# Kernel tuning notes

Hardware: AMD Instinct MI355X
Metric: run time of the kernel (lower is better)

The kernel has to match this reference:

```python
import jax, jax.numpy as jnp
import numpy as np

B, S, D = 4, 2048, 1024

def setup_inputs() -> dict:
    key = jax.random.key(0)
    k1, k2, k3, k4 = jax.random.split(key, 4)
    scale = 1.0 / np.sqrt(D)
    return {
        "X": jax.random.normal(k1, (B, S, D), dtype=jnp.float32),
        "W_Q": jax.random.normal(k2, (D, D), dtype=jnp.float32) * scale,
        "W_K": jax.random.normal(k3, (D, D), dtype=jnp.float32) * scale,
        "W_V": jax.random.normal(k4, (D, D), dtype=jnp.float32) * scale,
    }

def reference(X, W_Q, W_K, W_V):
    # nn.Linear computes X @ W.T; weights stored as [out, in]
    Q = jnp.einsum('bsd,ed->bse', X, W_Q)
    K = jnp.einsum('bsd,ed->bse', X, W_K)
    V = jnp.einsum('bsd,ed->bse', X, W_V)
    d_model = X.shape[-1]
    scores = jnp.einsum('bqd,bkd->bqk', Q, K) / jnp.sqrt(jnp.float32(d_model))
    S_len = X.shape[1]
    causal = jnp.tril(jnp.ones((S_len, S_len), dtype=bool))  # True = keep
    scores = jnp.where(causal[None, :, :], scores, -jnp.inf)
    attn = jax.nn.softmax(scores, axis=-1)
    return jnp.einsum('bqk,bkd->bqd', attn, V)
```

## Files before the change

### kernel.cpp

```cpp
#include <hip/hip_runtime.h>

typedef unsigned short u16;
typedef __attribute__((ext_vector_type(8))) short short8;
typedef __attribute__((ext_vector_type(4))) float floatx4;
typedef __attribute__((ext_vector_type(4))) unsigned short ushortx4;

#define BATCH 4
#define SEQ   2048
#define DMODEL 1024

__device__ __forceinline__ u16 f2bf(float f) {
  unsigned int u = __builtin_bit_cast(unsigned int, f);
  u = (u + 0x7FFFu + ((u >> 16) & 1u)) >> 16;
  return (u16)u;
}

typedef const __attribute__((address_space(1))) unsigned int as1_u32;
typedef __attribute__((address_space(3))) unsigned int as3_u32;

__device__ __forceinline__ void gload16(const void* gp, void* lp) {
  __builtin_amdgcn_global_load_lds((as1_u32*)gp, (as3_u32*)lp, 16, 0, 0);
}

#define CFENCE asm volatile("" ::: "memory")
#define LGKM0  do { asm volatile("s_waitcnt lgkmcnt(0)" ::: "memory"); \
                    __builtin_amdgcn_sched_barrier(0); } while (0)

template<int NW, int STRIPE>
__device__ __forceinline__ void stage_unit(
    const u16* __restrict__ G, int ld, int org, int kt, int h,
    u16* region, int w, int l)
{
  constexpr int CPS = STRIPE / 16;
  const int lr = l >> 3, s = l & 7;
  #pragma unroll
  for (int i = 0; i < 2; ++i) {
    int c = i * NW + w;
    int R = (c / CPS) * STRIPE + h * (STRIPE / 2) + (c % CPS) * 8;
    const u16* src = G + (size_t)(org + R + lr) * ld + kt * 64 + ((s ^ lr) << 3);
    gload16(src, region + R * 64);
  }
}

template<int REP>
__device__ __forceinline__ short8 rdfrag(const u16* region, int wq, int m, int kh, int l) {
  int r = wq * (REP * 16) + m * 16 + (l & 15);
  int c = kh * 32 + ((l >> 4) << 3);
  return *(const short8*)(region + ((r * 64 + c) ^ ((r & 7) << 3)));
}

template<int WM, int WN, int MREP, int NREP>
__device__ __forceinline__ void gemm_core(
    const u16* __restrict__ A, int lda,
    const u16* __restrict__ B, int ldb,
    int m0, int n0, int NT, u16* lds,
    floatx4 (&acc)[MREP][NREP])
{
  constexpr int NW = WM * WN;
  constexpr int BM = WM * MREP * 16, BN = WN * NREP * 16;
  constexpr int ABUF = BM * 64;
  constexpr int BUFSZ = (BM + BN) * 64;
  constexpr int MH = MREP / 2, NH = NREP / 2;
  constexpr int SA = BM / WM, SB = BN / WN;

  const int tid = threadIdx.x;
  const int w = tid >> 6, l = tid & 63;
  const int wr = w / WN, wc = w % WN;

  u16* buf0 = lds;
  u16* buf1 = lds + BUFSZ;

  stage_unit<NW, SA>(A, lda, m0, 0, 0, buf0, w, l);
  stage_unit<NW, SB>(B, ldb, n0, 0, 0, buf0 + ABUF, w, l);
  stage_unit<NW, SB>(B, ldb, n0, 0, 1, buf0 + ABUF, w, l);
  stage_unit<NW, SA>(A, lda, m0, 0, 1, buf0, w, l);
  stage_unit<NW, SA>(A, lda, m0, 1, 0, buf1, w, l);
  stage_unit<NW, SB>(B, ldb, n0, 1, 0, buf1 + ABUF, w, l);
  asm volatile("s_waitcnt vmcnt(8)" ::: "memory");
  __builtin_amdgcn_s_barrier();
  CFENCE;

  for (int kt = 0; kt < NT; ++kt) {
    u16* cur = (kt & 1) ? buf1 : buf0;
    u16* oth = (kt & 1) ? buf0 : buf1;
    const int t1 = (kt + 1 < NT) ? kt + 1 : NT - 1;
    const int t2 = (kt + 2 < NT) ? kt + 2 : NT - 1;

    short8 aLo[MH][2], aHi[MH][2], bLo[NH][2], bHi[NH][2];

    #pragma unroll
    for (int m = 0; m < MH; ++m)
      #pragma unroll
      for (int k = 0; k < 2; ++k) aLo[m][k] = rdfrag<MREP>(cur, wr, m, k, l);
    #pragma unroll
    for (int n = 0; n < NH; ++n)
      #pragma unroll
      for (int k = 0; k < 2; ++k) bLo[n][k] = rdfrag<NREP>(cur + ABUF, wc, n, k, l);
    stage_unit<NW, SB>(B, ldb, n0, t1, 1, oth + ABUF, w, l);
    stage_unit<NW, SA>(A, lda, m0, t1, 1, oth, w, l);
    asm volatile("s_waitcnt vmcnt(10)" ::: "memory");
    LGKM0;
    __builtin_amdgcn_s_barrier();
    CFENCE;
    __builtin_amdgcn_s_setprio(1);
    #pragma unroll
    for (int m = 0; m < MH; ++m)
      #pragma unroll
      for (int n = 0; n < NH; ++n)
        #pragma unroll
        for (int k = 0; k < 2; ++k)
          acc[m][n] = __builtin_amdgcn_mfma_f32_16x16x32_bf16(aLo[m][k], bLo[n][k], acc[m][n], 0, 0, 0);
    __builtin_amdgcn_s_setprio(0);

    #pragma unroll
    for (int n = 0; n < NH; ++n)
      #pragma unroll
      for (int k = 0; k < 2; ++k) bHi[n][k] = rdfrag<NREP>(cur + ABUF, wc, n + NH, k, l);
    stage_unit<NW, SA>(A, lda, m0, t2, 0, cur, w, l);
    asm volatile("s_waitcnt vmcnt(10)" ::: "memory");
    LGKM0;
    __builtin_amdgcn_s_barrier();
    CFENCE;
    __builtin_amdgcn_s_setprio(1);
    #pragma unroll
    for (int m = 0; m < MH; ++m)
      #pragma unroll
      for (int n = 0; n < NH; ++n)
        #pragma unroll
        for (int k = 0; k < 2; ++k)
          acc[m][n + NH] = __builtin_amdgcn_mfma_f32_16x16x32_bf16(aLo[m][k], bHi[n][k], acc[m][n + NH], 0, 0, 0);
    __builtin_amdgcn_s_setprio(0);

    #pragma unroll
    for (int m = 0; m < MH; ++m)
      #pragma unroll
      for (int k = 0; k < 2; ++k) aHi[m][k] = rdfrag<MREP>(cur, wr, m + MH, k, l);
    stage_unit<NW, SB>(B, ldb, n0, t2, 0, cur + ABUF, w, l);
    asm volatile("s_waitcnt vmcnt(8)" ::: "memory");
    LGKM0;
    __builtin_amdgcn_s_barrier();
    CFENCE;
    __builtin_amdgcn_s_setprio(1);
    #pragma unroll
    for (int m = 0; m < MH; ++m)
      #pragma unroll
      for (int n = 0; n < NH; ++n)
        #pragma unroll
        for (int k = 0; k < 2; ++k) {
          acc[m + MH][n + NH] = __builtin_amdgcn_mfma_f32_16x16x32_bf16(aHi[m][k], bHi[n][k], acc[m + MH][n + NH], 0, 0, 0);
          acc[m + MH][n] = __builtin_amdgcn_mfma_f32_16x16x32_bf16(aHi[m][k], bLo[n][k], acc[m + MH][n], 0, 0, 0);
        }
    __builtin_amdgcn_s_setprio(0);
  }
  asm volatile("s_waitcnt vmcnt(0)" ::: "memory");
}

__global__ __launch_bounds__(256)
void convert_k(const float* __restrict__ X,
               const float* __restrict__ WQ,
               const float* __restrict__ WK,
               const float* __restrict__ WV,
               u16* __restrict__ Xb, u16* __restrict__ Wb)
{
  const int NX = (BATCH*SEQ*DMODEL) / 4;
  const int NW_ = (DMODEL*DMODEL) / 4;
  const int total = NX + 3*NW_;
  for (int i = blockIdx.x * 256 + threadIdx.x; i < total; i += gridDim.x * 256) {
    const float4* src; u16* dst; int j;
    if (i < NX) { src = (const float4*)X; j = i; dst = Xb; }
    else {
      int t = i - NX; int w = t / NW_; j = t - w * NW_;
      src = (const float4*)(w == 0 ? WQ : (w == 1 ? WK : WV));
      dst = Wb + (size_t)w * (DMODEL*DMODEL);
    }
    float4 v = src[j];
    ushortx4 p = { f2bf(v.x), f2bf(v.y), f2bf(v.z), f2bf(v.w) };
    *(ushortx4*)(dst + (size_t)j * 4) = p;
  }
}

__global__ __launch_bounds__(512, 2)
void qk256(const u16* __restrict__ Xb, const u16* __restrict__ Wb,
           u16* __restrict__ Q, u16* __restrict__ K)
{
  __shared__ __align__(16) u16 lds[2 * (256 + 256) * 64];
  const int id = blockIdx.x;
  const int sw = (id & 7) * 32 + (id >> 3);
  const int z = sw >> 7;
  const int rem = sw & 127;
  const int mt = rem >> 2, nt = rem & 3;
  const int m0 = mt * 256, n0 = nt * 256;

  floatx4 acc[8][4] = {};
  gemm_core<2, 4, 8, 4>(Xb, DMODEL, Wb + (size_t)z * DMODEL * DMODEL, DMODEL,
                        m0, n0, DMODEL / 64, lds, acc);

  const int l = threadIdx.x & 63, w = threadIdx.x >> 6;
  const int wr = w >> 2, wc = w & 3;
  const int row0 = m0 + wr * 128 + ((l >> 4) << 2);
  const int col0 = n0 + wc * 64 + (l & 15);
  u16* O = z ? K : Q;
  #pragma unroll
  for (int m = 0; m < 8; ++m)
    #pragma unroll
    for (int n = 0; n < 4; ++n)
      #pragma unroll
      for (int i = 0; i < 4; ++i)
        O[(size_t)(row0 + m*16 + i) * DMODEL + col0 + n*16] = f2bf(acc[m][n][i]);
}

__global__ __launch_bounds__(256, 2)
void v128(const u16* __restrict__ Xb, const u16* __restrict__ Wb,
          u16* __restrict__ Vt)
{
  __shared__ __align__(16) u16 lds[2 * (128 + 128) * 64];
  const int id = blockIdx.x;
  const int sw = (id & 7) * 64 + (id >> 3);
  const int mt = sw >> 3, nt = sw & 7;
  const int m0 = mt * 128, n0 = nt * 128;

  floatx4 acc[4][4] = {};
  gemm_core<2, 2, 4, 4>(Xb, DMODEL, Wb + (size_t)2 * DMODEL * DMODEL, DMODEL,
                        m0, n0, DMODEL / 64, lds, acc);

  const int l = threadIdx.x & 63, w = threadIdx.x >> 6;
  const int wr = w >> 1, wc = w & 1;
  const int row0 = m0 + wr * 64 + ((l >> 4) << 2);
  const int col0 = n0 + wc * 64 + (l & 15);
  #pragma unroll
  for (int m = 0; m < 4; ++m) {
    int gm = row0 + m*16;
    int b = gm >> 11, s = gm & (SEQ - 1);
    #pragma unroll
    for (int n = 0; n < 4; ++n) {
      int d = col0 + n*16;
      ushortx4 p = { f2bf(acc[m][n][0]), f2bf(acc[m][n][1]),
                     f2bf(acc[m][n][2]), f2bf(acc[m][n][3]) };
      *(ushortx4*)(Vt + ((size_t)b * DMODEL + d) * SEQ + s) = p;
    }
  }
}

__global__ __launch_bounds__(256, 2)
void scores128(const u16* __restrict__ Qb, const u16* __restrict__ Kb,
               float* __restrict__ Sc)
{
  __shared__ __align__(16) u16 lds[2 * (128 + 128) * 64];
  const int id = blockIdx.x;
  const int sw = (id & 7) * 68 + (id >> 3);
  const int b = sw / 136;
  const int t = sw % 136;
  int qt = 0;
  while ((qt + 1) * (qt + 2) / 2 <= t) ++qt;
  const int kt = t - qt * (qt + 1) / 2;
  const int m0 = qt * 128, n0 = kt * 128;

  const u16* Q = Qb + (size_t)b * SEQ * DMODEL;
  const u16* K = Kb + (size_t)b * SEQ * DMODEL;
  floatx4 acc[4][4] = {};
  gemm_core<2, 2, 4, 4>(Q, DMODEL, K, DMODEL, m0, n0, DMODEL / 64, lds, acc);

  float* S = Sc + (size_t)b * SEQ * SEQ;
  const int l = threadIdx.x & 63, w = threadIdx.x >> 6;
  const int wr = w >> 1, wc = w & 1;
  const int row0 = m0 + wr * 64 + ((l >> 4) << 2);
  const int col0 = n0 + wc * 64 + (l & 15);
  #pragma unroll
  for (int m = 0; m < 4; ++m)
    #pragma unroll
    for (int n = 0; n < 4; ++n)
      #pragma unroll
      for (int i = 0; i < 4; ++i)
        S[(size_t)(row0 + m*16 + i) * SEQ + col0 + n*16] = acc[m][n][i] * 0.03125f;
}

__global__ __launch_bounds__(256)
void softmax_k(float* __restrict__ Sc)
{
  __shared__ float buf[SEQ];
  __shared__ float red[4];
  const int rg = blockIdx.x;
  const int q = rg & (SEQ - 1);
  float* row = Sc + (size_t)rg * SEQ;
  u16* prow = (u16*)row;
  const int tid = threadIdx.x;
  const int lane = tid & 63, wave = tid >> 6;
  const int n = q + 1;
  const int kpad = ((q >> 8) + 1) << 8;

  float lmax = -3.4e38f;
  for (int k = tid; k < n; k += 256) {
    float v = row[k];
    buf[k] = v;
    lmax = fmaxf(lmax, v);
  }
  #pragma unroll
  for (int off = 32; off >= 1; off >>= 1)
    lmax = fmaxf(lmax, __shfl_xor(lmax, off));
  if (lane == 0) red[wave] = lmax;
  __syncthreads();
  const float rmax = fmaxf(fmaxf(red[0], red[1]), fmaxf(red[2], red[3]));
  __syncthreads();

  float lsum = 0.f;
  for (int k = tid; k < n; k += 256) {
    float e = __expf(buf[k] - rmax);
    buf[k] = e;
    lsum += e;
  }
  #pragma unroll
  for (int off = 32; off >= 1; off >>= 1)
    lsum += __shfl_xor(lsum, off);
  if (lane == 0) red[wave] = lsum;
  __syncthreads();
  const float inv = 1.f / (red[0] + red[1] + red[2] + red[3]);

  for (int k = tid; k < kpad; k += 256) {
    float p = (k < n) ? buf[k] * inv : 0.f;
    prow[k] = f2bf(p);
  }
}

__global__ __launch_bounds__(256, 2)
void out128(const float* __restrict__ Sc, const u16* __restrict__ Vt,
            float* __restrict__ Out)
{
  __shared__ __align__(16) u16 lds[2 * (128 + 128) * 64];
  const int id = blockIdx.x;
  const int j = id & 255;
  const int upper = id >> 8;
  const int qt = upper ? (15 - (j & 15)) : (j & 15);
  const int nt = (j >> 4) & 7;
  const int b  = (upper << 1) | (j >> 7);
  const int m0 = qt * 128, n0 = nt * 128;

  const u16* P = (const u16*)(Sc + (size_t)b * SEQ * SEQ);
  const u16* V = Vt + (size_t)b * DMODEL * SEQ;
  const int NT = (qt + 1) * 2;

  floatx4 acc[4][4] = {};
  gemm_core<2, 2, 4, 4>(P, 2 * SEQ, V, SEQ, m0, n0, NT, lds, acc);

  float* O = Out + (size_t)b * SEQ * DMODEL;
  const int l = threadIdx.x & 63, w = threadIdx.x >> 6;
  const int wr = w >> 1, wc = w & 1;
  const int row0 = m0 + wr * 64 + ((l >> 4) << 2);
  const int col0 = n0 + wc * 64 + (l & 15);
  #pragma unroll
  for (int m = 0; m < 4; ++m)
    #pragma unroll
    for (int n = 0; n < 4; ++n)
      #pragma unroll
      for (int i = 0; i < 4; ++i)
        O[(size_t)(row0 + m*16 + i) * DMODEL + col0 + n*16] = acc[m][n][i];
}

extern "C" void kernel_launch(void* const* d_in, const int* in_sizes, int n_in,
                              void* d_out, int out_size, void* d_ws, size_t ws_size,
                              hipStream_t stream)
{
  const float* X  = (const float*)d_in[0];
  const float* WQ = (const float*)d_in[1];
  const float* WK = (const float*)d_in[2];
  const float* WV = (const float*)d_in[3];
  float* Out = (float*)d_out;

  char* ws = (char*)d_ws;
  u16*   Xb = (u16*)(ws);
  u16*   Wb = (u16*)(ws + 16777216);
  u16*   Qb = (u16*)(ws + 23068672);
  u16*   Kb = (u16*)(ws + 39845888);
  u16*   Vt = (u16*)(ws + 56623104);
  float* Sc = (float*)(ws + 73400320);

  convert_k<<<dim3(2048), dim3(256), 0, stream>>>(X, WQ, WK, WV, Xb, Wb);
  qk256<<<dim3(256), dim3(512), 0, stream>>>(Xb, Wb, Qb, Kb);
  v128<<<dim3(512), dim3(256), 0, stream>>>(Xb, Wb, Vt);
  scores128<<<dim3(544), dim3(256), 0, stream>>>(Qb, Kb, Sc);
  softmax_k<<<dim3(BATCH * SEQ), dim3(256), 0, stream>>>(Sc);
  out128<<<dim3(512), dim3(256), 0, stream>>>(Sc, Vt, Out);
}
```

Measured before the change: 143.6 us.

## Restructure GEMM main loop into two-tile unrolled, four-phase pipelined schedule

Result: no change. 145.2 us (+1.1%).

```diff
diff --git a/kernel.cpp b/kernel.cpp
--- a/kernel.cpp
+++ b/kernel.cpp
@@ -25,6 +25,10 @@
 #define CFENCE asm volatile("" ::: "memory")
 #define LGKM0  do { asm volatile("s_waitcnt lgkmcnt(0)" ::: "memory"); \
                     __builtin_amdgcn_sched_barrier(0); } while (0)
+#define VMC(n) asm volatile("s_waitcnt vmcnt(" #n ")" ::: "memory")
+#define BAR    __builtin_amdgcn_s_barrier()
+#define PRIO1  __builtin_amdgcn_s_setprio(1)
+#define PRIO0  __builtin_amdgcn_s_setprio(0)
 
 template<int NW, int STRIPE>
 __device__ __forceinline__ void stage_unit(
@@ -67,42 +71,38 @@
   const int w = tid >> 6, l = tid & 63;
   const int wr = w / WN, wc = w % WN;
 
-  u16* buf0 = lds;
-  u16* buf1 = lds + BUFSZ;
-
-  stage_unit<NW, SA>(A, lda, m0, 0, 0, buf0, w, l);
-  stage_unit<NW, SB>(B, ldb, n0, 0, 0, buf0 + ABUF, w, l);
-  stage_unit<NW, SB>(B, ldb, n0, 0, 1, buf0 + ABUF, w, l);
-  stage_unit<NW, SA>(A, lda, m0, 0, 1, buf0, w, l);
-  stage_unit<NW, SA>(A, lda, m0, 1, 0, buf1, w, l);
-  stage_unit<NW, SB>(B, ldb, n0, 1, 0, buf1 + ABUF, w, l);
-  asm volatile("s_waitcnt vmcnt(8)" ::: "memory");
-  __builtin_amdgcn_s_barrier();
+  u16* const bufp[2] = { lds, lds + BUFSZ };
+
+  stage_unit<NW, SA>(A, lda, m0, 0, 0, bufp[0], w, l);
+  stage_unit<NW, SB>(B, ldb, n0, 0, 0, bufp[0] + ABUF, w, l);
+  stage_unit<NW, SB>(B, ldb, n0, 0, 1, bufp[0] + ABUF, w, l);
+  stage_unit<NW, SA>(A, lda, m0, 0, 1, bufp[0], w, l);
+  stage_unit<NW, SA>(A, lda, m0, 1, 0, bufp[1], w, l);
+  stage_unit<NW, SB>(B, ldb, n0, 1, 0, bufp[1] + ABUF, w, l);
+  stage_unit<NW, SB>(B, ldb, n0, 1, 1, bufp[1] + ABUF, w, l);
+  VMC(6);
+  BAR;
   CFENCE;
 
-  for (int kt = 0; kt < NT; ++kt) {
-    u16* cur = (kt & 1) ? buf1 : buf0;
-    u16* oth = (kt & 1) ? buf0 : buf1;
-    const int t1 = (kt + 1 < NT) ? kt + 1 : NT - 1;
-    const int t2 = (kt + 2 < NT) ? kt + 2 : NT - 1;
+  for (int t = 0; t < NT; t += 2) {
+    u16* c0 = bufp[t & 1];
+    u16* c1 = bufp[(t + 1) & 1];
+    const int t2 = (t + 2 < NT) ? t + 2 : NT - 1;
+    const int t3 = (t + 3 < NT) ? t + 3 : NT - 1;
 
     short8 aLo[MH][2], aHi[MH][2], bLo[NH][2], bHi[NH][2];
 
     #pragma unroll
     for (int m = 0; m < MH; ++m)
       #pragma unroll
-      for (int k = 0; k < 2; ++k) aLo[m][k] = rdfrag<MREP>(cur, wr, m, k, l);
+      for (int k = 0; k < 2; ++k) aLo[m][k] = rdfrag<MREP>(c0, wr, m, k, l);
     #pragma unroll
     for (int n = 0; n < NH; ++n)
       #pragma unroll
-      for (int k = 0; k < 2; ++k) bLo[n][k] = rdfrag<NREP>(cur + ABUF, wc, n, k, l);
-    stage_unit<NW, SB>(B, ldb, n0, t1, 1, oth + ABUF, w, l);
-    stage_unit<NW, SA>(A, lda, m0, t1, 1, oth, w, l);
-    asm volatile("s_waitcnt vmcnt(10)" ::: "memory");
-    LGKM0;
-    __builtin_amdgcn_s_barrier();
-    CFENCE;
-    __builtin_amdgcn_s_setprio(1);
+      for (int k = 0; k < 2; ++k) bLo[n][k] = rdfrag<NREP>(c0 + ABUF, wc, n, k, l);
+    stage_unit<NW, SA>(A, lda, m0, t + 1, 1, c1, w, l);
+    if constexpr (MH * 2 + NH * 2 >= 12) asm volatile("s_waitcnt lgkmcnt(8)" ::: "memory");
+    BAR; LGKM0; PRIO1;
     #pragma unroll
     for (int m = 0; m < MH; ++m)
       #pragma unroll
@@ -110,18 +110,14 @@
         #pragma unroll
         for (int k = 0; k < 2; ++k)
           acc[m][n] = __builtin_amdgcn_mfma_f32_16x16x32_bf16(aLo[m][k], bLo[n][k], acc[m][n], 0, 0, 0);
-    __builtin_amdgcn_s_setprio(0);
+    PRIO0; BAR; CFENCE;
 
     #pragma unroll
     for (int n = 0; n < NH; ++n)
       #pragma unroll
-      for (int k = 0; k < 2; ++k) bHi[n][k] = rdfrag<NREP>(cur + ABUF, wc, n + NH, k, l);
-    stage_unit<NW, SA>(A, lda, m0, t2, 0, cur, w, l);
-    asm volatile("s_waitcnt vmcnt(10)" ::: "memory");
-    LGKM0;
-    __builtin_amdgcn_s_barrier();
-    CFENCE;
-    __builtin_amdgcn_s_setprio(1);
+      for (int k = 0; k < 2; ++k) bHi[n][k] = rdfrag<NREP>(c0 + ABUF, wc, n + NH, k, l);
+    stage_unit<NW, SA>(A, lda, m0, t2, 0, c0, w, l);
+    BAR; LGKM0; PRIO1;
     #pragma unroll
     for (int m = 0; m < MH; ++m)
       #pragma unroll
@@ -129,30 +125,98 @@
         #pragma unroll
         for (int k = 0; k < 2; ++k)
           acc[m][n + NH] = __builtin_amdgcn_mfma_f32_16x16x32_bf16(aLo[m][k], bHi[n][k], acc[m][n + NH], 0, 0, 0);
-    __builtin_amdgcn_s_setprio(0);
-
-    #pragma unroll
-    for (int m = 0; m < MH; ++m)
-      #pragma unroll
-      for (int k = 0; k < 2; ++k) aHi[m][k] = rdfrag<MREP>(cur, wr, m + MH, k, l);
-    stage_unit<NW, SB>(B, ldb, n0, t2, 0, cur + ABUF, w, l);
-    asm volatile("s_waitcnt vmcnt(8)" ::: "memory");
-    LGKM0;
-    __builtin_amdgcn_s_barrier();
-    CFENCE;
-    __builtin_amdgcn_s_setprio(1);
-    #pragma unroll
-    for (int m = 0; m < MH; ++m)
-      #pragma unroll
-      for (int n = 0; n < NH; ++n)
-        #pragma unroll
-        for (int k = 0; k < 2; ++k) {
+    PRIO0; BAR; CFENCE;
+
+    #pragma unroll
+    for (int m = 0; m < MH; ++m)
+      #pragma unroll
+      for (int k = 0; k < 2; ++k) aHi[m][k] = rdfrag<MREP>(c0, wr, m + MH, k, l);
+    stage_unit<NW, SB>(B, ldb, n0, t2, 0, c0 + ABUF, w, l);
+    BAR; LGKM0; PRIO1;
+    #pragma unroll
+    for (int m = 0; m < MH; ++m)
+      #pragma unroll
+      for (int n = 0; n < NH; ++n)
+        #pragma unroll
+        for (int k = 0; k < 2; ++k)
           acc[m + MH][n + NH] = __builtin_amdgcn_mfma_f32_16x16x32_bf16(aHi[m][k], bHi[n][k], acc[m + MH][n + NH], 0, 0, 0);
+    PRIO0; BAR; CFENCE;
+
+    stage_unit<NW, SB>(B, ldb, n0, t2, 1, c0 + ABUF, w, l);
+    VMC(6);
+    BAR; PRIO1;
+    #pragma unroll
+    for (int m = 0; m < MH; ++m)
+      #pragma unroll
+      for (int n = 0; n < NH; ++n)
+        #pragma unroll
+        for (int k = 0; k < 2; ++k)
           acc[m + MH][n] = __builtin_amdgcn_mfma_f32_16x16x32_bf16(aHi[m][k], bLo[n][k], acc[m + MH][n], 0, 0, 0);
-        }
-    __builtin_amdgcn_s_setprio(0);
-  }
-  asm volatile("s_waitcnt vmcnt(0)" ::: "memory");
+    PRIO0; BAR; CFENCE;
+
+    #pragma unroll
+    for (int m = 0; m < MH; ++m)
+      #pragma unroll
+      for (int k = 0; k < 2; ++k) aLo[m][k] = rdfrag<MREP>(c1, wr, m, k, l);
+    #pragma unroll
+    for (int n = 0; n < NH; ++n)
+      #pragma unroll
+      for (int k = 0; k < 2; ++k) bLo[n][k] = rdfrag<NREP>(c1 + ABUF, wc, n, k, l);
+    stage_unit<NW, SA>(A, lda, m0, t2, 1, c0, w, l);
+    if constexpr (MH * 2 + NH * 2 >= 12) asm volatile("s_waitcnt lgkmcnt(8)" ::: "memory");
+    BAR; LGKM0; PRIO1;
+    #pragma unroll
+    for (int m = 0; m < MH; ++m)
+      #pragma unroll
+      for (int n = 0; n < NH; ++n)
+        #pragma unroll
+        for (int k = 0; k < 2; ++k)
+          acc[m][n] = __builtin_amdgcn_mfma_f32_16x16x32_bf16(aLo[m][k], bLo[n][k], acc[m][n], 0, 0, 0);
+    PRIO0; BAR; CFENCE;
+
+    #pragma unroll
+    for (int n = 0; n < NH; ++n)
+      #pragma unroll
+      for (int k = 0; k < 2; ++k) bHi[n][k] = rdfrag<NREP>(c1 + ABUF, wc, n + NH, k, l);
+    stage_unit<NW, SA>(A, lda, m0, t3, 0, c1, w, l);
+    BAR; LGKM0; PRIO1;
+    #pragma unroll
+    for (int m = 0; m < MH; ++m)
+      #pragma unroll
+      for (int n = 0; n < NH; ++n)
+        #pragma unroll
+        for (int k = 0; k < 2; ++k)
+          acc[m][n + NH] = __builtin_amdgcn_mfma_f32_16x16x32_bf16(aLo[m][k], bHi[n][k], acc[m][n + NH], 0, 0, 0);
+    PRIO0; BAR; CFENCE;
+
+    #pragma unroll
+    for (int m = 0; m < MH; ++m)
+      #pragma unroll
+      for (int k = 0; k < 2; ++k) aHi[m][k] = rdfrag<MREP>(c1, wr, m + MH, k, l);
+    stage_unit<NW, SB>(B, ldb, n0, t3, 0, c1 + ABUF, w, l);
+    BAR; LGKM0; PRIO1;
+    #pragma unroll
+    for (int m = 0; m < MH; ++m)
+      #pragma unroll
+      for (int n = 0; n < NH; ++n)
+        #pragma unroll
+        for (int k = 0; k < 2; ++k)
+          acc[m + MH][n + NH] = __builtin_amdgcn_mfma_f32_16x16x32_bf16(aHi[m][k], bHi[n][k], acc[m + MH][n + NH], 0, 0, 0);
+    PRIO0; BAR; CFENCE;
+
+    stage_unit<NW, SB>(B, ldb, n0, t3, 1, c1 + ABUF, w, l);
+    VMC(6);
+    BAR; PRIO1;
+    #pragma unroll
+    for (int m = 0; m < MH; ++m)
+      #pragma unroll
+      for (int n = 0; n < NH; ++n)
+        #pragma unroll
+        for (int k = 0; k < 2; ++k)
+          acc[m + MH][n] = __builtin_amdgcn_mfma_f32_16x16x32_bf16(aHi[m][k], bLo[n][k], acc[m + MH][n], 0, 0, 0);
+    PRIO0; BAR; CFENCE;
+  }
+  VMC(0);
 }
 
 __global__ __launch_bounds__(256)
```
